# Optimization experiments

Hardware: AMD Instinct MI355X
Metric: run time of the kernel (lower is better)

Reference implementation:

```python
import jax, jax.numpy as jnp
import numpy as np

SIGMAS = (0.02, 0.01, 0.008)   # self.sig
SIGMA_N = 0.5                  # self.sig_n
COORD_SCALE = 0.05             # keep distances commensurate with sigmas


def setup_inputs() -> dict:
    key = jax.random.key(0)
    k1, k2, k3 = jax.random.split(key, 3)
    B, Vn, Fn = 2, 5000, 6144
    predictions = jax.random.uniform(k1, (B, Vn, 3), dtype=jnp.float32) * COORD_SCALE
    targets = jax.random.uniform(k2, (B, Vn, 3), dtype=jnp.float32) * COORD_SCALE
    faces = jax.random.randint(k3, (Fn, 3), 0, Vn, dtype=jnp.int32)
    return {"predictions": predictions, "targets": targets, "faces": faces}


def _mesh_quantities(V, F):
    # face centers C [F,3], areas L [F,1], unit normals Nn [F,3]
    v0, v1, v2 = V[F[:, 0]], V[F[:, 1]], V[F[:, 2]]
    C = (v0 + v1 + v2) / 3.0
    N = 0.5 * jnp.cross(v1 - v0, v2 - v0)
    L = jnp.sqrt((N * N).sum(-1, keepdims=True) + 1e-24)
    return C, L, N / L


def _varifold_prod(C1, L1, N1, C2, L2, N2, sigma, sigma_n):
    # <mu1, mu2> = sum_ij L1_i L2_j exp(-|c_i-c_j|^2/sigma^2) exp((<n_i,n_j>-1)/sigma_n^2)
    d2 = ((C1[:, None, :] - C2[None, :, :]) ** 2).sum(-1)          # [F,F]
    ndot = N1 @ N2.T                                               # [F,F]
    K = jnp.exp(-d2 / (sigma * sigma) + (ndot - 1.0) / (sigma_n * sigma_n))
    return (L1[:, 0] * (K @ L2[:, 0])).sum()


def reference(predictions, targets, faces):
    def per_sample(Vs, Vt):
        Cs, Ls, Ns = _mesh_quantities(Vs, faces)
        Ct, Lt, Nt = _mesh_quantities(Vt, faces)
        li = jnp.float32(0.0)
        for sig in SIGMAS:  # small fixed set of sigmas
            w = (sig / SIGMAS[0]) ** 2
            pss = _varifold_prod(Cs, Ls, Ns, Cs, Ls, Ns, sig, SIGMA_N)
            pst = _varifold_prod(Cs, Ls, Ns, Ct, Lt, Nt, sig, SIGMA_N)
            ptt = _varifold_prod(Ct, Lt, Nt, Ct, Lt, Nt, sig, SIGMA_N)
            li = li + w * (pss - 2.0 * pst + ptt)
        return li

    L = jax.vmap(per_sample)(predictions, targets)  # [B]
    return jnp.mean(L)
```

## Files before the change

kernel.cpp:

```cpp
#include <hip/hip_runtime.h>

#define F_FACES 6144
#define VN      5000

#define SC_F    30.02806022f
#define SN_F    2.40224481f
#define C4_F    5.7707801635558535f

typedef float v2f __attribute__((ext_vector_type(2)));

__device__ __forceinline__ float fast_exp2(float x) {
    float r; asm("v_exp_f32 %0, %1" : "=v"(r) : "v"(x)); return r;
}
__device__ __forceinline__ v2f pk_fma(v2f a, v2f b, v2f c) {
    return __builtin_elementwise_fma(a, b, c);
}

#define CELLS_OFF_FLOATS (4 * F_FACES * 2 * 4)

__global__ __launch_bounds__(256) void mesh_prep(
    const float* __restrict__ pred, const float* __restrict__ targ,
    const int* __restrict__ faces, float4* __restrict__ ws4,
    float* __restrict__ cells)
{
    const int f = blockIdx.x * 256 + threadIdx.x;
    const int m = blockIdx.y;
    if (blockIdx.x == 0 && m == 0 && threadIdx.x < 64)
        cells[threadIdx.x * 16] = 0.0f;
    if (f >= F_FACES) return;

    const int b = m >> 1, which = m & 1;
    const float* V = (which ? targ : pred) + b * (VN * 3);

    const int i0 = faces[3 * f + 0];
    const int i1 = faces[3 * f + 1];
    const int i2 = faces[3 * f + 2];

    const float v0x = V[3 * i0 + 0], v0y = V[3 * i0 + 1], v0z = V[3 * i0 + 2];
    const float v1x = V[3 * i1 + 0], v1y = V[3 * i1 + 1], v1z = V[3 * i1 + 2];
    const float v2x = V[3 * i2 + 0], v2y = V[3 * i2 + 1], v2z = V[3 * i2 + 2];

    const float Cx = (v0x + v1x + v2x) * (1.0f / 3.0f);
    const float Cy = (v0y + v1y + v2y) * (1.0f / 3.0f);
    const float Cz = (v0z + v1z + v2z) * (1.0f / 3.0f);

    const float e1x = v1x - v0x, e1y = v1y - v0y, e1z = v1z - v0z;
    const float e2x = v2x - v0x, e2y = v2y - v0y, e2z = v2z - v0z;

    const float Nx = 0.5f * (e1y * e2z - e1z * e2y);
    const float Ny = 0.5f * (e1z * e2x - e1x * e2z);
    const float Nz = 0.5f * (e1x * e2y - e1y * e2x);

    const float l2  = Nx * Nx + Ny * Ny + Nz * Nz + 1e-24f;
    const float L   = sqrtf(l2);
    const float inv = 1.0f / L;

    const float Csx = Cx * SC_F, Csy = Cy * SC_F, Csz = Cz * SC_F;
    const float a   = -(Csx * Csx + Csy * Csy + Csz * Csz);
    const float s   = inv * SN_F;

    const long base = (long)(m * F_FACES + f) * 2;
    ws4[base + 0] = make_float4(Csx, Csy, Csz, a);
    ws4[base + 1] = make_float4(Nx * s, Ny * s, Nz * s, log2f(L) - C4_F);
}

#define BLK       128
#define IT        4
#define KP        (IT / 2)
#define I_ROWS    (BLK * IT)
#define I_TILES   (F_FACES / I_ROWS)
#define W_TRI_Q   39936
#define TRI_TOTAL (4 * W_TRI_Q)
#define N_BLOCKS  12288
#define CPB       25

__global__ __launch_bounds__(BLK, 6) void varifold_pairs(
    const float4* __restrict__ ws4, float* __restrict__ cells)
{
    __shared__ float4 sAB[2 * CPB];
    __shared__ float  red[2];

    const int tid = threadIdx.x;
    int col = blockIdx.x * CPB;
    int remaining = CPB;
    float total = 0.0f;

    int cur_key = -1;
    v2f C2x2[KP], C2y2[KP], C2z2[KP], Ai2[KP];
    v2f Nix2[KP], Niy2[KP], Niz2[KP], Li2[KP];
    v2f acc2[KP];

    const v2f c025 = {0.25f, 0.25f};
    const v2f c016 = {0.16f, 0.16f};

    while (remaining > 0) {
        int c, b, it, j, r, bandLeft;
        if (col < TRI_TOTAL) {
            const int q = col / W_TRI_Q;
            r = col - q * W_TRI_Q;
            c = (q >> 1) ? 2 : 0; b = q & 1;
            it = 0;
            int w = F_FACES;
            while (r >= w) { r -= w; ++it; w -= I_ROWS; }
            j = it * I_ROWS + r;
            bandLeft = w - r;
        } else {
            const int lin = col - TRI_TOTAL;
            const int band = lin / F_FACES;
            r = lin - band * F_FACES;
            j = r;
            b = band / I_TILES; it = band - (band / I_TILES) * I_TILES;
            c = 1;
            bandLeft = F_FACES - r;
        }
        const bool strad = (c != 1) && (r < I_ROWS);
        int segLen = min(remaining, bandLeft);
        if (strad) segLen = min(segLen, I_ROWS - r);
        const float wOut = (c == 1) ? -1.0f : (strad ? 0.5f : 1.0f);
        const int m1 = 2 * b + (c == 2 ? 1 : 0);
        const int m2 = 2 * b + (c >= 1 ? 1 : 0);
        const float4* P1 = ws4 + (long)m1 * (F_FACES * 2);
        const float4* P2 = ws4 + (long)m2 * (F_FACES * 2);
        const int iBase = it * I_ROWS;

        const int key = m1 * 16 + it;
        if (key != cur_key) {
            cur_key = key;
#pragma unroll
            for (int kp = 0; kp < KP; ++kp) {
#pragma unroll
                for (int h = 0; h < 2; ++h) {
                    const int k = 2 * kp + h;
                    const int i = iBase + k * BLK + tid;
                    const float4 A  = P1[2 * i + 0];
                    const float4 Bv = P1[2 * i + 1];
                    C2x2[kp][h] = 2.0f * A.x;
                    C2y2[kp][h] = 2.0f * A.y;
                    C2z2[kp][h] = 2.0f * A.z;
                    Ai2[kp][h]  = A.w;
                    Nix2[kp][h] = Bv.x; Niy2[kp][h] = Bv.y; Niz2[kp][h] = Bv.z;
                    Li2[kp][h]  = fast_exp2(Bv.w + C4_F);
                }
            }
        }
#pragma unroll
        for (int kp = 0; kp < KP; ++kp) acc2[kp] = (v2f){0.0f, 0.0f};

        __syncthreads();
        if (tid < 2 * segLen) sAB[tid] = P2[2 * j + tid];
        __syncthreads();

        if (!strad) {
            for (int jj = 0; jj < segLen; ++jj) {
                const float4 a4 = sAB[2 * jj + 0];
                const float4 b4 = sAB[2 * jj + 1];
                const v2f axs = {a4.x, a4.x}, ays = {a4.y, a4.y};
                const v2f azs = {a4.z, a4.z}, aws = {a4.w, a4.w};
                const v2f bxs = {b4.x, b4.x}, bys = {b4.y, b4.y};
                const v2f bzs = {b4.z, b4.z}, bws = {b4.w, b4.w};
#pragma unroll
                for (int kp = 0; kp < KP; ++kp) {
                    v2f rr = pk_fma(C2x2[kp], axs, Ai2[kp]);
                    rr = pk_fma(C2y2[kp], ays, rr);
                    rr = pk_fma(C2z2[kp], azs, rr);
                    rr = rr + aws;
                    const v2f t0 = {fast_exp2(rr.x), fast_exp2(rr.y)};
                    v2f n = pk_fma(Nix2[kp], bxs, bws);
                    n = pk_fma(Niy2[kp], bys, n);
                    n = pk_fma(Niz2[kp], bzs, n);
                    const v2f en = {fast_exp2(n.x), fast_exp2(n.y)};
                    const v2f t2  = t0 * t0;
                    const v2f t4  = t2 * t2;
                    const v2f t8  = t4 * t4;
                    const v2f t16 = t8 * t8;
                    const v2f t24 = t16 * t8;
                    const v2f t25 = t24 * t0;
                    v2f p = pk_fma(c025, t16, t4);
                    p = pk_fma(c016, t25, p);
                    acc2[kp] = pk_fma(en, p, acc2[kp]);
                }
            }
        } else {
            for (int jj = 0; jj < segLen; ++jj) {
                const float4 a4 = sAB[2 * jj + 0];
                const float4 b4 = sAB[2 * jj + 1];
                const int jg = j + jj;
                const v2f axs = {a4.x, a4.x}, ays = {a4.y, a4.y};
                const v2f azs = {a4.z, a4.z}, aws = {a4.w, a4.w};
                const v2f bxs = {b4.x, b4.x}, bys = {b4.y, b4.y};
                const v2f bzs = {b4.z, b4.z}, bws = {b4.w, b4.w};
#pragma unroll
                for (int kp = 0; kp < KP; ++kp) {
                    v2f rr = pk_fma(C2x2[kp], axs, Ai2[kp]);
                    rr = pk_fma(C2y2[kp], ays, rr);
                    rr = pk_fma(C2z2[kp], azs, rr);
                    rr = rr + aws;
                    const v2f t0 = {fast_exp2(rr.x), fast_exp2(rr.y)};
                    v2f n = pk_fma(Nix2[kp], bxs, bws);
                    n = pk_fma(Niy2[kp], bys, n);
                    n = pk_fma(Niz2[kp], bzs, n);
                    v2f en = {fast_exp2(n.x), fast_exp2(n.y)};
                    const int i0 = iBase + (2 * kp + 0) * BLK + tid;
                    const int i1 = iBase + (2 * kp + 1) * BLK + tid;
                    float f0 = (jg > i0) ? 2.0f : 0.0f; f0 = (jg == i0) ? 1.0f : f0;
                    float f1 = (jg > i1) ? 2.0f : 0.0f; f1 = (jg == i1) ? 1.0f : f1;
                    const v2f fw = {f0, f1};
                    en = en * fw;
                    const v2f t2  = t0 * t0;
                    const v2f t4  = t2 * t2;
                    const v2f t8  = t4 * t4;
                    const v2f t16 = t8 * t8;
                    const v2f t24 = t16 * t8;
                    const v2f t25 = t24 * t0;
                    v2f p = pk_fma(c025, t16, t4);
                    p = pk_fma(c016, t25, p);
                    acc2[kp] = pk_fma(en, p, acc2[kp]);
                }
            }
        }

        float part = 0.0f;
#pragma unroll
        for (int kp = 0; kp < KP; ++kp) {
            part = fmaf(acc2[kp].x, Li2[kp].x, part);
            part = fmaf(acc2[kp].y, Li2[kp].y, part);
        }
        total = fmaf(wOut, part, total);

        col += segLen; remaining -= segLen;
    }

#pragma unroll
    for (int off = 32; off; off >>= 1) total += __shfl_xor(total, off);
    if ((tid & 63) == 0) red[tid >> 6] = total;
    __syncthreads();
    if (tid == 0)
        atomicAdd(&cells[(blockIdx.x & 63) * 16], red[0] + red[1]);
}

__global__ __launch_bounds__(64) void finalize_sum(
    const float* __restrict__ cells, float* __restrict__ out)
{
    float v = cells[threadIdx.x * 16];
#pragma unroll
    for (int off = 32; off; off >>= 1) v += __shfl_xor(v, off);
    if (threadIdx.x == 0) out[0] = v;
}

extern "C" void kernel_launch(void* const* d_in, const int* in_sizes, int n_in,
                              void* d_out, int out_size, void* d_ws, size_t ws_size,
                              hipStream_t stream) {
    const float* pred  = (const float*)d_in[0];
    const float* targ  = (const float*)d_in[1];
    const int*   faces = (const int*)d_in[2];
    float*       out   = (float*)d_out;
    float4*      ws4   = (float4*)d_ws;
    float*       cells = (float*)d_ws + CELLS_OFF_FLOATS;

    dim3 g1(F_FACES / 256, 4);
    mesh_prep<<<g1, 256, 0, stream>>>(pred, targ, faces, ws4, cells);

    varifold_pairs<<<dim3(N_BLOCKS), dim3(BLK), 0, stream>>>(ws4, cells);

    finalize_sum<<<dim3(1), dim3(64), 0, stream>>>(cells, out);
}
```

Before: 124.4 us.

## Double rows per thread and pre-splat shared column data into packed pairs

Each thread now holds eight i-rows instead of four, so every column read from shared memory is reused across more rows. Work per block (CPB) and the triangle quota are rescaled to match, and occupancy is lowered to four blocks per SIMD. Column data is also stored in shared memory already duplicated into v2f pairs, which removes the register moves that built broadcast vectors for the packed FMAs. The larger register footprint may reduce latency hiding and the coarser work split may hurt load balance.

```diff
diff --git a/kernel.cpp b/kernel.cpp
--- a/kernel.cpp
+++ b/kernel.cpp
@@ -65,19 +65,19 @@
 }
 
 #define BLK       128
-#define IT        4
+#define IT        8
 #define KP        (IT / 2)
 #define I_ROWS    (BLK * IT)
 #define I_TILES   (F_FACES / I_ROWS)
-#define W_TRI_Q   39936
+#define W_TRI_Q   21504
 #define TRI_TOTAL (4 * W_TRI_Q)
 #define N_BLOCKS  12288
-#define CPB       25
-
-__global__ __launch_bounds__(BLK, 6) void varifold_pairs(
+#define CPB       13
+
+__global__ __launch_bounds__(BLK, 4) void varifold_pairs(
     const float4* __restrict__ ws4, float* __restrict__ cells)
 {
-    __shared__ float4 sAB[2 * CPB];
+    __shared__ float4 sD4[CPB * 4];
     __shared__ float  red[2];
 
     const int tid = threadIdx.x;
@@ -147,17 +147,22 @@
         for (int kp = 0; kp < KP; ++kp) acc2[kp] = (v2f){0.0f, 0.0f};
 
         __syncthreads();
-        if (tid < 2 * segLen) sAB[tid] = P2[2 * j + tid];
+        if (tid < 2 * segLen) {
+            const int face = tid >> 1, half = tid & 1;
+            const float4 v = P2[2 * (j + face) + half];
+            sD4[face * 4 + half * 2 + 0] = make_float4(v.x, v.x, v.y, v.y);
+            sD4[face * 4 + half * 2 + 1] = make_float4(v.z, v.z, v.w, v.w);
+        }
         __syncthreads();
+
+        const v2f* sV = (const v2f*)sD4;
 
         if (!strad) {
             for (int jj = 0; jj < segLen; ++jj) {
-                const float4 a4 = sAB[2 * jj + 0];
-                const float4 b4 = sAB[2 * jj + 1];
-                const v2f axs = {a4.x, a4.x}, ays = {a4.y, a4.y};
-                const v2f azs = {a4.z, a4.z}, aws = {a4.w, a4.w};
-                const v2f bxs = {b4.x, b4.x}, bys = {b4.y, b4.y};
-                const v2f bzs = {b4.z, b4.z}, bws = {b4.w, b4.w};
+                const v2f axs = sV[8 * jj + 0], ays = sV[8 * jj + 1];
+                const v2f azs = sV[8 * jj + 2], aws = sV[8 * jj + 3];
+                const v2f bxs = sV[8 * jj + 4], bys = sV[8 * jj + 5];
+                const v2f bzs = sV[8 * jj + 6], bws = sV[8 * jj + 7];
 #pragma unroll
                 for (int kp = 0; kp < KP; ++kp) {
                     v2f rr = pk_fma(C2x2[kp], axs, Ai2[kp]);
@@ -182,13 +187,11 @@
             }
         } else {
             for (int jj = 0; jj < segLen; ++jj) {
-                const float4 a4 = sAB[2 * jj + 0];
-                const float4 b4 = sAB[2 * jj + 1];
+                const v2f axs = sV[8 * jj + 0], ays = sV[8 * jj + 1];
+                const v2f azs = sV[8 * jj + 2], aws = sV[8 * jj + 3];
+                const v2f bxs = sV[8 * jj + 4], bys = sV[8 * jj + 5];
+                const v2f bzs = sV[8 * jj + 6], bws = sV[8 * jj + 7];
                 const int jg = j + jj;
-                const v2f axs = {a4.x, a4.x}, ays = {a4.y, a4.y};
-                const v2f azs = {a4.z, a4.z}, aws = {a4.w, a4.w};
-                const v2f bxs = {b4.x, b4.x}, bys = {b4.y, b4.y};
-                const v2f bzs = {b4.z, b4.z}, bws = {b4.w, b4.w};
 #pragma unroll
                 for (int kp = 0; kp < KP; ++kp) {
                     v2f rr = pk_fma(C2x2[kp], axs, Ai2[kp]);
```

After: 136.4 us. 1.1x slower.
